# Optimization experiments

Hardware: AMD Instinct MI355X
Metric: run time of the kernel (lower is better)

Reference implementation:

```python
import jax, jax.numpy as jnp
import numpy as np
from jax import lax

D = 2048          # latent_dim
H = 4096          # hrm_hidden_dim
K = 4             # hrm_update_interval
MAX_STEPS = 16    # hrm_max_steps
MOM = 0.9         # hrm_momentum
THR = 0.01        # hrm_convergence_threshold


def _gru(x, h, wih, whh, bih, bhh):
    # torch.nn.GRUCell math; gate order r, z, n
    gi = wih @ x + bih          # (3*hidden,)
    gh = whh @ h + bhh
    ir, iz, inn = jnp.split(gi, 3)
    hr, hz, hn = jnp.split(gh, 3)
    r = jax.nn.sigmoid(ir + hr)
    z = jax.nn.sigmoid(iz + hz)
    n = jnp.tanh(inn + r * hn)
    return (1.0 - z) * n + z * h


def setup_inputs() -> dict:
    key = jax.random.key(0)
    ks = jax.random.split(key, 24)
    def U(k, shape, fan):
        s = 1.0 / np.sqrt(fan)
        return jax.random.uniform(k, shape, jnp.float32, -s, s)
    return {
        "query": jax.random.normal(ks[0], (D,), jnp.float32),
        "h_gru_wih": U(ks[1], (3 * H, 2 * D), H),
        "h_gru_whh": U(ks[2], (3 * H, H), H),
        "h_gru_bih": U(ks[3], (3 * H,), H),
        "h_gru_bhh": U(ks[4], (3 * H,), H),
        "l_gru_wih": U(ks[5], (3 * D, D), D),
        "l_gru_whh": U(ks[6], (3 * D, D), D),
        "l_gru_bih": U(ks[7], (3 * D,), D),
        "l_gru_bhh": U(ks[8], (3 * D,), D),
        "h_dir_w": U(ks[9], (D, H), H),
        "h_dir_b": U(ks[10], (D,), H),
        "h_conv_w": U(ks[11], (1, H), H),
        "h_conv_b": U(ks[12], (1,), H),
        "l_out_w": U(ks[13], (D, D), D),
        "l_out_b": U(ks[14], (D,), D),
        "halt_w": U(ks[15], (1, H + D), H + D),
        "halt_b": U(ks[16], (1,), H + D),
        "reset_w": U(ks[17], (1, H + D + 1), H + D + 1),
        "reset_b": U(ks[18], (1,), H + D + 1),
        "l_init_w": U(ks[19], (D, H), H),
        "l_init_b": U(ks[20], (D,), H),
    }


def _forward(query, h_gru_wih, h_gru_whh, h_gru_bih, h_gru_bhh,
             l_gru_wih, l_gru_whh, l_gru_bih, l_gru_bhh,
             h_dir_w, h_dir_b, h_conv_w, h_conv_b,
             l_out_w, l_out_b, halt_w, halt_b,
             reset_w, reset_b, l_init_w, l_init_b):
    q = query[:D]

    def step(carry, step_idx):
        h, l, cum, result, weight, best, mom, active = carry
        # H-module update every K steps (only while active)
        do_h = active & (step_idx % K == 0)
        h = jnp.where(do_h,
                      _gru(jnp.concatenate([q, l]), h,
                           h_gru_wih, h_gru_whh, h_gru_bih, h_gru_bhh),
                      h)
        directive = jnp.tanh(h_dir_w @ h + h_dir_b)
        # raw_conv uses .item() in torch -> no gradient flows through it
        raw_conv = lax.stop_gradient(jax.nn.sigmoid(h_conv_w @ h + h_conv_b)[0])
        mom = jnp.where(active, MOM * mom + (1.0 - MOM) * raw_conv, mom)
        conv = mom
        # L-module update every step (only while active)
        l = jnp.where(active,
                      _gru(directive, l, l_gru_wih, l_gru_whh, l_gru_bih, l_gru_bhh),
                      l)
        res = jnp.tanh(l_out_w @ l + l_out_b)
        halt = jax.nn.sigmoid(halt_w @ jnp.concatenate([h, l]) + halt_b)[0]
        p = jnp.where(active, jnp.minimum(halt, 1.0 - cum), 0.0)
        result = result + p * res
        weight = weight + p
        cum = cum + p
        best = jnp.where(active & (conv > best + THR), conv, best)
        break_now = cum > 0.95
        # learned reset (skipped on the breaking step, and only for step > K)
        reset_prob = jax.nn.sigmoid(
            reset_w @ jnp.concatenate([h, l, conv[None]]) + reset_b)[0]
        do_reset = active & (~break_now) & (reset_prob > 0.7) & (step_idx > K)
        l = jnp.where(do_reset, jnp.tanh(l_init_w @ h + l_init_b), l)
        active = active & (~break_now)
        return (h, l, cum, result, weight, best, mom, active), None

    carry0 = (jnp.zeros(H, jnp.float32), jnp.zeros(D, jnp.float32),
              jnp.float32(0.0), jnp.zeros(D, jnp.float32), jnp.float32(0.0),
              jnp.float32(0.0), jnp.float32(0.0), jnp.array(True))
    (h, l, cum, result, weight, best, mom, active), _ = lax.scan(
        step, carry0, jnp.arange(MAX_STEPS))
    # result_weight > 0 always (p > 0 on step 0), so take the normalized path
    return result / jnp.maximum(weight, 1e-8)


def reference(query, h_gru_wih, h_gru_whh, h_gru_bih, h_gru_bhh,
              l_gru_wih, l_gru_whh, l_gru_bih, l_gru_bhh,
              h_dir_w, h_dir_b, h_conv_w, h_conv_b,
              l_out_w, l_out_b, halt_w, halt_b,
              reset_w, reset_b, l_init_w, l_init_b):
    return _forward(query, h_gru_wih, h_gru_whh, h_gru_bih, h_gru_bhh,
                    l_gru_wih, l_gru_whh, l_gru_bih, l_gru_bhh,
                    h_dir_w, h_dir_b, h_conv_w, h_conv_b,
                    l_out_w, l_out_b, halt_w, halt_b,
                    reset_w, reset_b, l_init_w, l_init_b)
```

## Files before the change

kernel.cpp:

```cpp
#include <hip/hip_runtime.h>
#include <math.h>

#define DD 2048
#define HH 4096
#define NSTEPS 16
#define KK 4

#define OFF_CAT    0
#define OFF_GI_H   6400
#define OFF_GH_H   18688
#define OFF_GI_L   30976
#define OFF_GH_L   37120
#define OFF_DIR    43264
#define OFF_RES    45312
#define OFF_RESULT 47360
#define OFF_SCAL   49408
#define OFF_BAR    49440
#define OFF_XCAT   49472

static __device__ __forceinline__ float sigf(float x) { return 1.0f / (1.0f + expf(-x)); }

static __device__ __forceinline__ float wred(float s) {
#pragma unroll
  for (int off = 32; off; off >>= 1) s += __shfl_down(s, off);
  return s;
}

static __device__ __forceinline__ float dot8(const float4* __restrict__ Wr,
                                             const float4* __restrict__ x,
                                             int n4, int lane) {
  float a0 = 0.f, a1 = 0.f, a2 = 0.f, a3 = 0.f;
  for (int i = lane; i + 448 < n4; i += 512) {
    float4 w0 = Wr[i],       w1 = Wr[i + 64],  w2 = Wr[i + 128], w3 = Wr[i + 192];
    float4 w4 = Wr[i + 256], w5 = Wr[i + 320], w6 = Wr[i + 384], w7 = Wr[i + 448];
    float4 v0 = x[i],        v1 = x[i + 64],   v2 = x[i + 128],  v3 = x[i + 192];
    float4 v4 = x[i + 256],  v5 = x[i + 320],  v6 = x[i + 384],  v7 = x[i + 448];
    a0 = fmaf(w0.x, v0.x, a0); a0 = fmaf(w0.y, v0.y, a0); a0 = fmaf(w0.z, v0.z, a0); a0 = fmaf(w0.w, v0.w, a0);
    a1 = fmaf(w1.x, v1.x, a1); a1 = fmaf(w1.y, v1.y, a1); a1 = fmaf(w1.z, v1.z, a1); a1 = fmaf(w1.w, v1.w, a1);
    a2 = fmaf(w2.x, v2.x, a2); a2 = fmaf(w2.y, v2.y, a2); a2 = fmaf(w2.z, v2.z, a2); a2 = fmaf(w2.w, v2.w, a2);
    a3 = fmaf(w3.x, v3.x, a3); a3 = fmaf(w3.y, v3.y, a3); a3 = fmaf(w3.z, v3.z, a3); a3 = fmaf(w3.w, v3.w, a3);
    a0 = fmaf(w4.x, v4.x, a0); a0 = fmaf(w4.y, v4.y, a0); a0 = fmaf(w4.z, v4.z, a0); a0 = fmaf(w4.w, v4.w, a0);
    a1 = fmaf(w5.x, v5.x, a1); a1 = fmaf(w5.y, v5.y, a1); a1 = fmaf(w5.z, v5.z, a1); a1 = fmaf(w5.w, v5.w, a1);
    a2 = fmaf(w6.x, v6.x, a2); a2 = fmaf(w6.y, v6.y, a2); a2 = fmaf(w6.z, v6.z, a2); a2 = fmaf(w6.w, v6.w, a2);
    a3 = fmaf(w7.x, v7.x, a3); a3 = fmaf(w7.y, v7.y, a3); a3 = fmaf(w7.z, v7.z, a3); a3 = fmaf(w7.w, v7.w, a3);
  }
  return wred((a0 + a1) + (a2 + a3));
}

static __device__ __forceinline__ void gsync(unsigned* bar, unsigned* gen,
                                             unsigned nblk, unsigned& lg) {
  __syncthreads();
  if (threadIdx.x == 0) {
    __threadfence();
    unsigned arrived = __hip_atomic_fetch_add(bar, 1u, __ATOMIC_ACQ_REL,
                                              __HIP_MEMORY_SCOPE_AGENT);
    if (arrived == nblk - 1) {
      __hip_atomic_store(bar, 0u, __ATOMIC_RELAXED, __HIP_MEMORY_SCOPE_AGENT);
      __hip_atomic_fetch_add(gen, 1u, __ATOMIC_ACQ_REL, __HIP_MEMORY_SCOPE_AGENT);
    } else {
      while (__hip_atomic_load(gen, __ATOMIC_ACQUIRE, __HIP_MEMORY_SCOPE_AGENT) == lg) {
        __builtin_amdgcn_s_sleep(2);
      }
    }
    lg++;
    __threadfence();
  }
  __syncthreads();
}

__global__ __launch_bounds__(256) void k_gi(
    const float* __restrict__ W, const float* __restrict__ b,
    const float4* __restrict__ x, float* __restrict__ y,
    int rows, int stride4, int n4, const float* __restrict__ gate) {
  if (gate && *gate == 0.0f) return;
  int row = (int)((blockIdx.x * 256 + threadIdx.x) >> 6);
  if (row >= rows) return;
  int lane = threadIdx.x & 63;
  float s = dot8((const float4*)W + (size_t)row * stride4, x, n4, lane);
  if (lane == 0) y[row] = s + b[row];
}

__global__ __launch_bounds__(256) void s0_hcombine(
    const float* __restrict__ gi, const float* __restrict__ bhh,
    float* __restrict__ cat, const float* __restrict__ query,
    float* __restrict__ xcat, unsigned* __restrict__ bar) {
  int i = blockIdx.x * 256 + threadIdx.x;
  if (i < HH) {
    float r = sigf(gi[i] + bhh[i]);
    float z = sigf(gi[HH + i] + bhh[HH + i]);
    float n = tanhf(gi[2 * HH + i] + r * bhh[2 * HH + i]);
    cat[i] = (1.0f - z) * n;
  }
  if (i < DD) xcat[i] = query[i];
  if (i < 2) bar[i] = 0u;
}

__global__ __launch_bounds__(256) void k_dir_conv(
    const float* __restrict__ dir_w, const float* __restrict__ dir_b,
    const float* __restrict__ conv_w, const float* __restrict__ halt_w,
    const float* __restrict__ cat, float* __restrict__ dirv,
    float* __restrict__ scal) {
  int w = (int)((blockIdx.x * 256 + threadIdx.x) >> 6);
  int lane = threadIdx.x & 63;
  if (w < DD) {
    float s = dot8((const float4*)dir_w + (size_t)w * 1024, (const float4*)cat, 1024, lane);
    if (lane == 0) dirv[w] = tanhf(s + dir_b[w]);
  } else if (w == DD) {
    float s = dot8((const float4*)conv_w, (const float4*)cat, 1024, lane);
    if (lane == 0) scal[8] = s;
  } else if (w == DD + 1) {
    float s = dot8((const float4*)halt_w, (const float4*)cat, 1024, lane);
    if (lane == 0) scal[9] = s;
  }
}

__global__ __launch_bounds__(1024) void s0_B(
    const float* __restrict__ gi_l, const float* __restrict__ l_bhh,
    float* __restrict__ cat, float* __restrict__ xcat,
    const float* __restrict__ conv_b, const float* __restrict__ halt_w,
    const float* __restrict__ halt_b, float* __restrict__ scal) {
  __shared__ float red[16];
  int tid = threadIdx.x, lane = tid & 63, wib = tid >> 6;
  for (int i = tid; i < DD; i += 1024) {
    float r = sigf(gi_l[i] + l_bhh[i]);
    float z = sigf(gi_l[DD + i] + l_bhh[DD + i]);
    float n = tanhf(gi_l[2 * DD + i] + r * l_bhh[2 * DD + i]);
    float lv = (1.0f - z) * n;
    cat[HH + i] = lv;
    xcat[DD + i] = lv;
  }
  __syncthreads();
  float s = 0.f;
  for (int i = tid; i < DD; i += 1024) s += halt_w[HH + i] * cat[HH + i];
  s = wred(s);
  if (lane == 0) red[wib] = s;
  __syncthreads();
  if (tid == 0) {
    float hl = 0.f;
#pragma unroll
    for (int k = 0; k < 16; k++) hl += red[k];
    float raw = sigf(scal[8] + conv_b[0]);
    scal[6] = raw;
    scal[3] = 0.1f * raw;
    float halt = sigf(scal[9] + hl + halt_b[0]);
    float p = fminf(halt, 1.0f);
    scal[7] = p;
    scal[1] = p;
    scal[0] = p;
    scal[4] = (p > 0.95f) ? 0.0f : 1.0f;
    scal[5] = 0.0f;
    scal[2] = 0.0f;
  }
}

__global__ __launch_bounds__(1024) void s1_B(
    const float* __restrict__ gi_l, const float* __restrict__ gh_l,
    float* __restrict__ cat, float* __restrict__ xcat,
    const float* __restrict__ halt_b, const float* __restrict__ halt_w,
    float* __restrict__ scal) {
  __shared__ float red[16];
  int tid = threadIdx.x, lane = tid & 63, wib = tid >> 6;
  if (scal[4] == 0.0f) {
    if (tid == 0) scal[7] = 0.0f;
    return;
  }
  for (int i = tid; i < DD; i += 1024) {
    float r = sigf(gi_l[i] + gh_l[i]);
    float z = sigf(gi_l[DD + i] + gh_l[DD + i]);
    float n = tanhf(gi_l[2 * DD + i] + r * gh_l[2 * DD + i]);
    float lv = (1.0f - z) * n + z * cat[HH + i];
    cat[HH + i] = lv;
    xcat[DD + i] = lv;
  }
  __syncthreads();
  float s = 0.f;
  for (int i = tid; i < DD; i += 1024) s += halt_w[HH + i] * cat[HH + i];
  s = wred(s);
  if (lane == 0) red[wib] = s;
  __syncthreads();
  if (tid == 0) {
    float hl = 0.f;
#pragma unroll
    for (int k = 0; k < 16; k++) hl += red[k];
    scal[3] = 0.9f * scal[3] + 0.1f * scal[6];
    float halt = sigf(scal[9] + hl + halt_b[0]);
    float cum = scal[0];
    float p = fminf(halt, 1.0f - cum);
    scal[7] = p;
    scal[1] += p;
    cum += p;
    scal[0] = cum;
    scal[4] = (cum > 0.95f) ? 0.0f : 1.0f;
  }
}

__global__ __launch_bounds__(256) void k_res_accum(
    const float* __restrict__ out_w, const float* __restrict__ out_b,
    const float* __restrict__ cat, float* __restrict__ result,
    const float* __restrict__ scal, int assign) {
  float p = scal[7];
  if (!assign && p == 0.0f) return;
  int row = (int)((blockIdx.x * 256 + threadIdx.x) >> 6);
  if (row >= DD) return;
  int lane = threadIdx.x & 63;
  float s = dot8((const float4*)out_w + (size_t)row * 512,
                 (const float4*)(cat + HH), 512, lane);
  if (lane == 0) {
    float r = tanhf(s + out_b[row]);
    result[row] = assign ? p * r : result[row] + p * r;
  }
}

__global__ __launch_bounds__(256) void k_out(
    const float* __restrict__ result, const float* __restrict__ scal,
    float* __restrict__ out) {
  int i = blockIdx.x * 256 + threadIdx.x;
  if (i < DD) out[i] = result[i] / fmaxf(scal[1], 1e-8f);
}

__global__ __launch_bounds__(256, 2) void k_rest(
    const float* __restrict__ h_wih, const float* __restrict__ h_whh,
    const float* __restrict__ h_bih, const float* __restrict__ h_bhh,
    const float* __restrict__ l_wih, const float* __restrict__ l_whh,
    const float* __restrict__ l_bih, const float* __restrict__ l_bhh,
    const float* __restrict__ dir_w, const float* __restrict__ dir_b,
    const float* __restrict__ conv_w, const float* __restrict__ conv_b,
    const float* __restrict__ out_w, const float* __restrict__ out_b,
    const float* __restrict__ halt_w, const float* __restrict__ halt_b,
    const float* __restrict__ reset_w, const float* __restrict__ reset_b,
    const float* __restrict__ init_w, const float* __restrict__ init_b,
    float* __restrict__ ws, unsigned nblk) {
  const int tid = threadIdx.x, lane = tid & 63, wib = tid >> 6;
  const int nw = (int)(gridDim.x << 2);
  const int wid = (int)((blockIdx.x << 2) | wib);
  const int gtid = (int)(blockIdx.x * 256 + tid);
  const int gsz = (int)(gridDim.x * 256);
  float* cat = ws + OFF_CAT;
  float* gi_h = ws + OFF_GI_H;
  float* gh_h = ws + OFF_GH_H;
  float* gi_l = ws + OFF_GI_L;
  float* gh_l = ws + OFF_GH_L;
  float* dir = ws + OFF_DIR;
  float* res = ws + OFF_RES;
  float* result = ws + OFF_RESULT;
  float* scal = ws + OFF_SCAL;
  float* xcat = ws + OFF_XCAT;
  unsigned* bar = (unsigned*)(ws + OFF_BAR);
  volatile float* vs = scal;
  unsigned lg = 0;

  for (int step = 2; step < NSTEPS; ++step) {
    if (vs[4] == 0.0f) break;
    const bool hstep = ((step & 3) == 0);
    if (hstep) {
      for (int r = wid; r < 6 * HH; r += nw) {
        if (r < 3 * HH) {
          float s = dot8((const float4*)h_wih + (size_t)r * 1024,
                         (const float4*)xcat, 1024, lane);
          if (lane == 0) gi_h[r] = s + h_bih[r];
        } else {
          int rr = r - 3 * HH;
          float s = dot8((const float4*)h_whh + (size_t)rr * 1024,
                         (const float4*)cat, 1024, lane);
          if (lane == 0) gh_h[rr] = s + h_bhh[rr];
        }
      }
      gsync(bar, bar + 1, nblk, lg);
      for (int i = gtid; i < HH; i += gsz) {
        float rr = sigf(gi_h[i] + gh_h[i]);
        float z = sigf(gi_h[HH + i] + gh_h[HH + i]);
        float nn = tanhf(gi_h[2 * HH + i] + rr * gh_h[2 * HH + i]);
        cat[i] = (1.0f - z) * nn + z * cat[i];
      }
      gsync(bar, bar + 1, nblk, lg);
      for (int r = wid; r < DD; r += nw) {
        float s = dot8((const float4*)dir_w + (size_t)r * 1024,
                       (const float4*)cat, 1024, lane);
        if (lane == 0) dir[r] = tanhf(s + dir_b[r]);
      }
      gsync(bar, bar + 1, nblk, lg);
    }
    {
      const int tot = hstep ? 12288 : 6144;
      for (int r = wid; r < tot; r += nw) {
        if (r < 6144) {
          float s = dot8((const float4*)l_whh + (size_t)r * 512,
                         (const float4*)(cat + HH), 512, lane);
          if (lane == 0) gh_l[r] = s + l_bhh[r];
        } else {
          int rr = r - 6144;
          float s = dot8((const float4*)l_wih + (size_t)rr * 512,
                         (const float4*)dir, 512, lane);
          if (lane == 0) gi_l[rr] = s + l_bih[rr];
        }
      }
    }
    gsync(bar, bar + 1, nblk, lg);
    for (int i = gtid; i < DD; i += gsz) {
      float rr = sigf(gi_l[i] + gh_l[i]);
      float z = sigf(gi_l[DD + i] + gh_l[DD + i]);
      float nn = tanhf(gi_l[2 * DD + i] + rr * gh_l[2 * DD + i]);
      float lv = (1.0f - z) * nn + z * cat[HH + i];
      cat[HH + i] = lv;
      xcat[DD + i] = lv;
    }
    gsync(bar, bar + 1, nblk, lg);
    for (int r = wid; r < DD; r += nw) {
      float s = dot8((const float4*)out_w + (size_t)r * 512,
                     (const float4*)(cat + HH), 512, lane);
      if (lane == 0) res[r] = tanhf(s + out_b[r]);
    }
    gsync(bar, bar + 1, nblk, lg);
    if (blockIdx.x == 0) {
      __shared__ float red[4];
      __shared__ float s_p;
      float s = 0.f;
      if (wib == 0) {
        if (hstep) {
          for (int i = lane; i < HH; i += 64) s += conv_w[i] * cat[i];
          s = wred(s);
          if (lane == 0) red[0] = s;
        }
      } else if (wib == 1) {
        for (int i = lane; i < HH + DD; i += 64) s += halt_w[i] * cat[i];
        s = wred(s);
        if (lane == 0) red[1] = s;
      } else if (wib == 2) {
        for (int i = lane; i < HH + DD; i += 64) s += reset_w[i] * cat[i];
        s = wred(s);
        if (lane == 0) red[2] = s;
      }
      __syncthreads();
      if (tid == 0) {
        float raw = hstep ? sigf(red[0] + conv_b[0]) : scal[6];
        if (hstep) scal[6] = raw;
        float mom = 0.9f * scal[3] + 0.1f * raw;
        scal[3] = mom;
        float halt = sigf(red[1] + halt_b[0]);
        float cum = scal[0];
        float p = fminf(halt, 1.0f - cum);
        scal[1] += p;
        cum += p;
        scal[0] = cum;
        bool brk = cum > 0.95f;
        float rdot = red[2] + reset_w[HH + DD] * mom + reset_b[0];
        scal[5] = (!brk && (sigf(rdot) > 0.7f) && (step > KK)) ? 1.0f : 0.0f;
        scal[4] = brk ? 0.0f : 1.0f;
        s_p = p;
      }
      __syncthreads();
      float p = s_p;
      for (int i = tid; i < DD; i += 256) result[i] += p * res[i];
      __threadfence();
    }
    gsync(bar, bar + 1, nblk, lg);
    if (step > KK && vs[5] != 0.0f) {
      for (int r = wid; r < DD; r += nw) {
        float s = dot8((const float4*)init_w + (size_t)r * 1024,
                       (const float4*)cat, 1024, lane);
        if (lane == 0) {
          float lv = tanhf(s + init_b[r]);
          cat[HH + r] = lv;
          xcat[DD + r] = lv;
        }
      }
      gsync(bar, bar + 1, nblk, lg);
    }
  }
}

extern "C" void kernel_launch(void* const* d_in, const int* in_sizes, int n_in,
                              void* d_out, int out_size, void* d_ws, size_t ws_size,
                              hipStream_t stream) {
  const float* query   = (const float*)d_in[0];
  const float* h_wih   = (const float*)d_in[1];
  const float* h_whh   = (const float*)d_in[2];
  const float* h_bih   = (const float*)d_in[3];
  const float* h_bhh   = (const float*)d_in[4];
  const float* l_wih   = (const float*)d_in[5];
  const float* l_whh   = (const float*)d_in[6];
  const float* l_bih   = (const float*)d_in[7];
  const float* l_bhh   = (const float*)d_in[8];
  const float* dir_w   = (const float*)d_in[9];
  const float* dir_b   = (const float*)d_in[10];
  const float* conv_w  = (const float*)d_in[11];
  const float* conv_b  = (const float*)d_in[12];
  const float* out_w   = (const float*)d_in[13];
  const float* out_b   = (const float*)d_in[14];
  const float* halt_w  = (const float*)d_in[15];
  const float* halt_b  = (const float*)d_in[16];
  const float* reset_w = (const float*)d_in[17];
  const float* reset_b = (const float*)d_in[18];
  const float* init_w  = (const float*)d_in[19];
  const float* init_b  = (const float*)d_in[20];

  float* ws = (float*)d_ws;
  float* out = (float*)d_out;
  float* cat = ws + OFF_CAT;
  float* gi_h = ws + OFF_GI_H;
  float* gi_l = ws + OFF_GI_L;
  float* gh_l = ws + OFF_GH_L;
  float* dir = ws + OFF_DIR;
  float* result = ws + OFF_RESULT;
  float* scal = ws + OFF_SCAL;
  float* xcat = ws + OFF_XCAT;
  unsigned* bar = (unsigned*)(ws + OFF_BAR);
  float* g_act = scal + 4;

  const float4* q4 = (const float4*)query;
  const float4* h4 = (const float4*)cat;
  const float4* l4 = (const float4*)(cat + HH);
  const float4* d4 = (const float4*)dir;

  k_gi<<<3072, 256, 0, stream>>>(h_wih, h_bih, q4, gi_h, 12288, 1024, 512,
                                 (const float*)nullptr);
  s0_hcombine<<<16, 256, 0, stream>>>(gi_h, h_bhh, cat, query, xcat, bar);
  k_dir_conv<<<513, 256, 0, stream>>>(dir_w, dir_b, conv_w, halt_w, cat, dir, scal);
  k_gi<<<1536, 256, 0, stream>>>(l_wih, l_bih, d4, gi_l, 6144, 512, 512,
                                 (const float*)nullptr);
  s0_B<<<1, 1024, 0, stream>>>(gi_l, l_bhh, cat, xcat, conv_b, halt_w, halt_b, scal);
  k_res_accum<<<512, 256, 0, stream>>>(out_w, out_b, cat, result, scal, 1);

  k_gi<<<1536, 256, 0, stream>>>(l_whh, l_bhh, l4, gh_l, 6144, 512, 512, g_act);
  s1_B<<<1, 1024, 0, stream>>>(gi_l, gh_l, cat, xcat, halt_b, halt_w, scal);
  k_res_accum<<<512, 256, 0, stream>>>(out_w, out_b, cat, result, scal, 0);

  int maxb = 0;
  if (hipOccupancyMaxActiveBlocksPerMultiprocessor(&maxb, k_rest, 256, 0) != hipSuccess)
    maxb = 1;
  unsigned nblk = (maxb >= 2) ? 512u : 256u;
  k_rest<<<nblk, 256, 0, stream>>>(h_wih, h_whh, h_bih, h_bhh,
                                   l_wih, l_whh, l_bih, l_bhh,
                                   dir_w, dir_b, conv_w, conv_b,
                                   out_w, out_b, halt_w, halt_b,
                                   reset_w, reset_b, init_w, init_b,
                                   ws, nblk);

  k_out<<<8, 256, 0, stream>>>(result, scal, out);
}
```

Before: 70.76 us.

## Fuse step-0 output GEMV with step-1 GRU GEMV and fold final normalize into persistent kernel

Step 0's output projection now runs in the same launch as step 1's hidden-hidden GEMV, since both read the same l vector. The weighted result is then combined later inside the persistent kernel using stored p0 and p1 scalars. The separate result-accumulate and output-normalize kernels are removed and the query copy moves into the first GEMV kernel, cutting launches on the serial critical path. It also adds a spin limit to the grid barrier, which guards against hangs but could break synchronization silently.

```diff
diff --git a/kernel.cpp b/kernel.cpp
--- a/kernel.cpp
+++ b/kernel.cpp
@@ -17,6 +17,7 @@
 #define OFF_SCAL   49408
 #define OFF_BAR    49440
 #define OFF_XCAT   49472
+#define OFF_RES2   53568
 
 static __device__ __forceinline__ float sigf(float x) { return 1.0f / (1.0f + expf(-x)); }
 
@@ -58,8 +59,10 @@
       __hip_atomic_store(bar, 0u, __ATOMIC_RELAXED, __HIP_MEMORY_SCOPE_AGENT);
       __hip_atomic_fetch_add(gen, 1u, __ATOMIC_ACQ_REL, __HIP_MEMORY_SCOPE_AGENT);
     } else {
+      long spins = 0;
       while (__hip_atomic_load(gen, __ATOMIC_ACQUIRE, __HIP_MEMORY_SCOPE_AGENT) == lg) {
         __builtin_amdgcn_s_sleep(2);
+        if (++spins > (1L << 24)) break;
       }
     }
     lg++;
@@ -67,23 +70,24 @@
   }
   __syncthreads();
 }
-
-__global__ __launch_bounds__(256) void k_gi(
-    const float* __restrict__ W, const float* __restrict__ b,
-    const float4* __restrict__ x, float* __restrict__ y,
-    int rows, int stride4, int n4, const float* __restrict__ gate) {
-  if (gate && *gate == 0.0f) return;
-  int row = (int)((blockIdx.x * 256 + threadIdx.x) >> 6);
-  if (row >= rows) return;
+#define GBAR gsync(bar, bar + 1, nblk, lg)
+
+__global__ __launch_bounds__(256) void kA_gih(
+    const float* __restrict__ h_wih, const float* __restrict__ h_bih,
+    const float* __restrict__ query, float* __restrict__ gi_h,
+    float* __restrict__ xcat) {
+  int gt = blockIdx.x * 256 + threadIdx.x;
+  if (gt < DD) xcat[gt] = query[gt];
+  int row = gt >> 6;
+  if (row >= 3 * HH) return;
   int lane = threadIdx.x & 63;
-  float s = dot8((const float4*)W + (size_t)row * stride4, x, n4, lane);
-  if (lane == 0) y[row] = s + b[row];
+  float s = dot8((const float4*)h_wih + (size_t)row * 1024, (const float4*)query, 512, lane);
+  if (lane == 0) gi_h[row] = s + h_bih[row];
 }
 
 __global__ __launch_bounds__(256) void s0_hcombine(
     const float* __restrict__ gi, const float* __restrict__ bhh,
-    float* __restrict__ cat, const float* __restrict__ query,
-    float* __restrict__ xcat, unsigned* __restrict__ bar) {
+    float* __restrict__ cat, unsigned* __restrict__ bar) {
   int i = blockIdx.x * 256 + threadIdx.x;
   if (i < HH) {
     float r = sigf(gi[i] + bhh[i]);
@@ -91,7 +95,6 @@
     float n = tanhf(gi[2 * HH + i] + r * bhh[2 * HH + i]);
     cat[i] = (1.0f - z) * n;
   }
-  if (i < DD) xcat[i] = query[i];
   if (i < 2) bar[i] = 0u;
 }
 
@@ -114,6 +117,16 @@
   }
 }
 
+__global__ __launch_bounds__(256) void kC_gil(
+    const float* __restrict__ l_wih, const float* __restrict__ l_bih,
+    const float* __restrict__ dir, float* __restrict__ gi_l) {
+  int row = (int)((blockIdx.x * 256 + threadIdx.x) >> 6);
+  if (row >= 3 * DD) return;
+  int lane = threadIdx.x & 63;
+  float s = dot8((const float4*)l_wih + (size_t)row * 512, (const float4*)dir, 512, lane);
+  if (lane == 0) gi_l[row] = s + l_bih[row];
+}
+
 __global__ __launch_bounds__(1024) void s0_B(
     const float* __restrict__ gi_l, const float* __restrict__ l_bhh,
     float* __restrict__ cat, float* __restrict__ xcat,
@@ -144,12 +157,31 @@
     scal[3] = 0.1f * raw;
     float halt = sigf(scal[9] + hl + halt_b[0]);
     float p = fminf(halt, 1.0f);
-    scal[7] = p;
+    scal[10] = p;
+    scal[11] = 0.0f;
     scal[1] = p;
     scal[0] = p;
     scal[4] = (p > 0.95f) ? 0.0f : 1.0f;
     scal[5] = 0.0f;
-    scal[2] = 0.0f;
+  }
+}
+
+__global__ __launch_bounds__(256) void kDE_pool(
+    const float* __restrict__ l_whh, const float* __restrict__ l_bhh,
+    const float* __restrict__ out_w, const float* __restrict__ out_b,
+    const float* __restrict__ cat, float* __restrict__ gh_l,
+    float* __restrict__ res) {
+  int t = (int)((blockIdx.x * 256 + threadIdx.x) >> 6);
+  if (t >= 8192) return;
+  int lane = threadIdx.x & 63;
+  const float4* l04 = (const float4*)(cat + HH);
+  if (t < 6144) {
+    float s = dot8((const float4*)l_whh + (size_t)t * 512, l04, 512, lane);
+    if (lane == 0) gh_l[t] = s + l_bhh[t];
+  } else {
+    int r = t - 6144;
+    float s = dot8((const float4*)out_w + (size_t)r * 512, l04, 512, lane);
+    if (lane == 0) res[r] = tanhf(s + out_b[r]);
   }
 }
 
@@ -160,10 +192,7 @@
     float* __restrict__ scal) {
   __shared__ float red[16];
   int tid = threadIdx.x, lane = tid & 63, wib = tid >> 6;
-  if (scal[4] == 0.0f) {
-    if (tid == 0) scal[7] = 0.0f;
-    return;
-  }
+  if (scal[4] == 0.0f) return;
   for (int i = tid; i < DD; i += 1024) {
     float r = sigf(gi_l[i] + gh_l[i]);
     float z = sigf(gi_l[DD + i] + gh_l[DD + i]);
@@ -186,7 +215,7 @@
     float halt = sigf(scal[9] + hl + halt_b[0]);
     float cum = scal[0];
     float p = fminf(halt, 1.0f - cum);
-    scal[7] = p;
+    scal[11] = p;
     scal[1] += p;
     cum += p;
     scal[0] = cum;
@@ -194,31 +223,20 @@
   }
 }
 
-__global__ __launch_bounds__(256) void k_res_accum(
+__global__ __launch_bounds__(256) void kE_res1(
     const float* __restrict__ out_w, const float* __restrict__ out_b,
-    const float* __restrict__ cat, float* __restrict__ result,
-    const float* __restrict__ scal, int assign) {
-  float p = scal[7];
-  if (!assign && p == 0.0f) return;
+    const float* __restrict__ cat, float* __restrict__ res2,
+    const float* __restrict__ p1gate) {
+  if (*p1gate == 0.0f) return;
   int row = (int)((blockIdx.x * 256 + threadIdx.x) >> 6);
   if (row >= DD) return;
   int lane = threadIdx.x & 63;
   float s = dot8((const float4*)out_w + (size_t)row * 512,
                  (const float4*)(cat + HH), 512, lane);
-  if (lane == 0) {
-    float r = tanhf(s + out_b[row]);
-    result[row] = assign ? p * r : result[row] + p * r;
-  }
-}
-
-__global__ __launch_bounds__(256) void k_out(
-    const float* __restrict__ result, const float* __restrict__ scal,
-    float* __restrict__ out) {
-  int i = blockIdx.x * 256 + threadIdx.x;
-  if (i < DD) out[i] = result[i] / fmaxf(scal[1], 1e-8f);
-}
-
-__global__ __launch_bounds__(256, 2) void k_rest(
+  if (lane == 0) res2[row] = tanhf(s + out_b[row]);
+}
+
+__global__ __launch_bounds__(256, 2) void kF_rest(
     const float* __restrict__ h_wih, const float* __restrict__ h_whh,
     const float* __restrict__ h_bih, const float* __restrict__ h_bhh,
     const float* __restrict__ l_wih, const float* __restrict__ l_whh,
@@ -229,7 +247,7 @@
     const float* __restrict__ halt_w, const float* __restrict__ halt_b,
     const float* __restrict__ reset_w, const float* __restrict__ reset_b,
     const float* __restrict__ init_w, const float* __restrict__ init_b,
-    float* __restrict__ ws, unsigned nblk) {
+    float* __restrict__ ws, float* __restrict__ out, unsigned nblk) {
   const int tid = threadIdx.x, lane = tid & 63, wib = tid >> 6;
   const int nw = (int)(gridDim.x << 2);
   const int wid = (int)((blockIdx.x << 2) | wib);
@@ -242,6 +260,7 @@
   float* gh_l = ws + OFF_GH_L;
   float* dir = ws + OFF_DIR;
   float* res = ws + OFF_RES;
+  float* res2 = ws + OFF_RES2;
   float* result = ws + OFF_RESULT;
   float* scal = ws + OFF_SCAL;
   float* xcat = ws + OFF_XCAT;
@@ -249,6 +268,23 @@
   volatile float* vs = scal;
   unsigned lg = 0;
 
+  float p0v = vs[10], p1v = vs[11];
+  if (vs[4] == 0.0f) {
+    float wgt = fmaxf(vs[1], 1e-8f);
+    for (int i = gtid; i < DD; i += gsz) {
+      float acc = p0v * res[i];
+      if (p1v != 0.0f) acc += p1v * res2[i];
+      out[i] = acc / wgt;
+    }
+    return;
+  }
+
+  for (int i = gtid; i < DD; i += gsz) {
+    float acc = p0v * res[i];
+    if (p1v != 0.0f) acc += p1v * res2[i];
+    result[i] = acc;
+  }
+  GBAR;
   for (int step = 2; step < NSTEPS; ++step) {
     if (vs[4] == 0.0f) break;
     const bool hstep = ((step & 3) == 0);
@@ -265,20 +301,20 @@
           if (lane == 0) gh_h[rr] = s + h_bhh[rr];
         }
       }
-      gsync(bar, bar + 1, nblk, lg);
+      GBAR;
       for (int i = gtid; i < HH; i += gsz) {
         float rr = sigf(gi_h[i] + gh_h[i]);
         float z = sigf(gi_h[HH + i] + gh_h[HH + i]);
         float nn = tanhf(gi_h[2 * HH + i] + rr * gh_h[2 * HH + i]);
         cat[i] = (1.0f - z) * nn + z * cat[i];
       }
-      gsync(bar, bar + 1, nblk, lg);
+      GBAR;
       for (int r = wid; r < DD; r += nw) {
         float s = dot8((const float4*)dir_w + (size_t)r * 1024,
                        (const float4*)cat, 1024, lane);
         if (lane == 0) dir[r] = tanhf(s + dir_b[r]);
       }
-      gsync(bar, bar + 1, nblk, lg);
+      GBAR;
     }
     {
       const int tot = hstep ? 12288 : 6144;
@@ -295,7 +331,7 @@
         }
       }
     }
-    gsync(bar, bar + 1, nblk, lg);
+    GBAR;
     for (int i = gtid; i < DD; i += gsz) {
       float rr = sigf(gi_l[i] + gh_l[i]);
       float z = sigf(gi_l[DD + i] + gh_l[DD + i]);
@@ -304,13 +340,13 @@
       cat[HH + i] = lv;
       xcat[DD + i] = lv;
     }
-    gsync(bar, bar + 1, nblk, lg);
+    GBAR;
     for (int r = wid; r < DD; r += nw) {
       float s = dot8((const float4*)out_w + (size_t)r * 512,
                      (const float4*)(cat + HH), 512, lane);
       if (lane == 0) res[r] = tanhf(s + out_b[r]);
     }
-    gsync(bar, bar + 1, nblk, lg);
+    GBAR;
     if (blockIdx.x == 0) {
       __shared__ float red[4];
       __shared__ float s_p;
@@ -353,7 +389,7 @@
       for (int i = tid; i < DD; i += 256) result[i] += p * res[i];
       __threadfence();
     }
-    gsync(bar, bar + 1, nblk, lg);
+    GBAR;
     if (step > KK && vs[5] != 0.0f) {
       for (int r = wid; r < DD; r += nw) {
         float s = dot8((const float4*)init_w + (size_t)r * 1024,
@@ -364,9 +400,11 @@
           xcat[DD + r] = lv;
         }
       }
-      gsync(bar, bar + 1, nblk, lg);
-    }
-  }
+      GBAR;
+    }
+  }
+  float wgt = fmaxf(vs[1], 1e-8f);
+  for (int i = gtid; i < DD; i += gsz) out[i] = result[i] / wgt;
 }
 
 extern "C" void kernel_launch(void* const* d_in, const int* in_sizes, int n_in,
@@ -396,45 +434,33 @@
 
   float* ws = (float*)d_ws;
   float* out = (float*)d_out;
-  float* cat = ws + OFF_CAT;
+  float* cat  = ws + OFF_CAT;
   float* gi_h = ws + OFF_GI_H;
   float* gi_l = ws + OFF_GI_L;
   float* gh_l = ws + OFF_GH_L;
-  float* dir = ws + OFF_DIR;
-  float* result = ws + OFF_RESULT;
+  float* dir  = ws + OFF_DIR;
+  float* res  = ws + OFF_RES;
+  float* res2 = ws + OFF_RES2;
   float* scal = ws + OFF_SCAL;
   float* xcat = ws + OFF_XCAT;
   unsigned* bar = (unsigned*)(ws + OFF_BAR);
-  float* g_act = scal + 4;
-
-  const float4* q4 = (const float4*)query;
-  const float4* h4 = (const float4*)cat;
-  const float4* l4 = (const float4*)(cat + HH);
-  const float4* d4 = (const float4*)dir;
-
-  k_gi<<<3072, 256, 0, stream>>>(h_wih, h_bih, q4, gi_h, 12288, 1024, 512,
-                                 (const float*)nullptr);
-  s0_hcombine<<<16, 256, 0, stream>>>(gi_h, h_bhh, cat, query, xcat, bar);
+
+  kA_gih<<<3072, 256, 0, stream>>>(h_wih, h_bih, query, gi_h, xcat);
+  s0_hcombine<<<16, 256, 0, stream>>>(gi_h, h_bhh, cat, bar);
   k_dir_conv<<<513, 256, 0, stream>>>(dir_w, dir_b, conv_w, halt_w, cat, dir, scal);
-  k_gi<<<1536, 256, 0, stream>>>(l_wih, l_bih, d4, gi_l, 6144, 512, 512,
-                                 (const float*)nullptr);
+  kC_gil<<<1536, 256, 0, stream>>>(l_wih, l_bih, dir, gi_l);
   s0_B<<<1, 1024, 0, stream>>>(gi_l, l_bhh, cat, xcat, conv_b, halt_w, halt_b, scal);
-  k_res_accum<<<512, 256, 0, stream>>>(out_w, out_b, cat, result, scal, 1);
-
-  k_gi<<<1536, 256, 0, stream>>>(l_whh, l_bhh, l4, gh_l, 6144, 512, 512, g_act);
+  kDE_pool<<<2048, 256, 0, stream>>>(l_whh, l_bhh, out_w, out_b, cat, gh_l, res);
   s1_B<<<1, 1024, 0, stream>>>(gi_l, gh_l, cat, xcat, halt_b, halt_w, scal);
-  k_res_accum<<<512, 256, 0, stream>>>(out_w, out_b, cat, result, scal, 0);
-
+  kE_res1<<<512, 256, 0, stream>>>(out_w, out_b, cat, res2, scal + 11);
   int maxb = 0;
-  if (hipOccupancyMaxActiveBlocksPerMultiprocessor(&maxb, k_rest, 256, 0) != hipSuccess)
+  if (hipOccupancyMaxActiveBlocksPerMultiprocessor(&maxb, kF_rest, 256, 0) != hipSuccess)
     maxb = 1;
   unsigned nblk = (maxb >= 2) ? 512u : 256u;
-  k_rest<<<nblk, 256, 0, stream>>>(h_wih, h_whh, h_bih, h_bhh,
-                                   l_wih, l_whh, l_bih, l_bhh,
-                                   dir_w, dir_b, conv_w, conv_b,
-                                   out_w, out_b, halt_w, halt_b,
-                                   reset_w, reset_b, init_w, init_b,
-                                   ws, nblk);
-
-  k_out<<<8, 256, 0, stream>>>(result, scal, out);
-}
+  kF_rest<<<nblk, 256, 0, stream>>>(h_wih, h_whh, h_bih, h_bhh,
+                                    l_wih, l_whh, l_bih, l_bhh,
+                                    dir_w, dir_b, conv_w, conv_b,
+                                    out_w, out_b, halt_w, halt_b,
+                                    reset_w, reset_b, init_w, init_b,
+                                    ws, out, nblk);
+}
```

Result: faster. 67.92 us (-4.0%).
